# Kernel tuning notes

Hardware: AMD Instinct MI355X
Metric: run time of the kernel (lower is better)

## Reference

```python
import jax, jax.numpy as jnp
import numpy as np

IN_DIM = 256   # opt.word_vec_size
MEM_DIM = 256  # opt.rnn_size // num_directions
N_LEAVES = 131072  # 2**17, complete binary tree


def setup_inputs() -> dict:
    key = jax.random.key(0)
    ks = jax.random.split(key, 8)
    s = 0.05  # weight scale
    return {
        # leaf word2vec embeddings, in-order leaf sequence of the tree
        "x": jax.random.normal(ks[0], (N_LEAVES, IN_DIM), jnp.float32),
        # BinaryTreeLeafModule params (Linear as x @ W + b)
        "Wcx": jax.random.normal(ks[1], (IN_DIM, MEM_DIM), jnp.float32) * s,
        "bcx": jnp.zeros((MEM_DIM,), jnp.float32),
        "Wox": jax.random.normal(ks[2], (IN_DIM, MEM_DIM), jnp.float32) * s,
        "box": jnp.zeros((MEM_DIM,), jnp.float32),
        # BinaryTreeComposer params: 4 left-child gates (i, lf, rf, u) fused
        # along the output dim, likewise 4 right-child gates.
        "Wl": jax.random.normal(ks[3], (MEM_DIM, 4 * MEM_DIM), jnp.float32) * s,
        "bl": jnp.zeros((4 * MEM_DIM,), jnp.float32),
        "Wr": jax.random.normal(ks[4], (MEM_DIM, 4 * MEM_DIM), jnp.float32) * s,
        "br": jnp.zeros((4 * MEM_DIM,), jnp.float32),
        "lengths": N_LEAVES,  # max sequence length for output padding
    }


def reference(x, Wcx, bcx, Wox, box, Wl, bl, Wr, br, lengths):
    m = Wcx.shape[1]
    # ---- BinaryTreeLeafModule, batched over all leaves ----
    c = x @ Wcx + bcx                                   # [n, m]
    h = jax.nn.sigmoid(x @ Wox + box) * jnp.tanh(c)     # [n, m]
    leaf_h = h  # in-order cat of leaf outputs == recursive cat([lo, ro])

    # ---- BinaryTreeComposer, one batched step per tree level ----
    # Loop over log2(n_leaves) levels of a complete binary tree; each
    # iteration composes adjacent sibling pairs (shapes static -> jit-safe).
    while c.shape[0] > 1:
        lc, rc = c[0::2], c[1::2]
        lh, rh = h[0::2], h[1::2]
        g = (lh @ Wl + bl) + (rh @ Wr + br)             # [n/2, 4m]
        gi, glf, grf, gu = jnp.split(g, 4, axis=-1)
        i = jax.nn.sigmoid(gi)
        lf = jax.nn.sigmoid(glf)
        rf = jax.nn.sigmoid(grf)
        u = jnp.tanh(gu)
        c = i * u + lf * lc + rf * rc                   # [n/2, m]
        h = jnp.tanh(c)                                 # gate_output=False

    # ---- root post-processing (as in original when tree.parent is None) ----
    output = leaf_h[:, None, :]                         # [n_leaves, 1, m]
    supl = int(lengths) - output.shape[0]
    if supl > 0:
        output = jnp.concatenate(
            [output, jnp.zeros((supl, 1, m), output.dtype)], axis=0)
    c_root = c[:, None, :]                              # [1, 1, m]
    h_root = h[:, None, :]                              # [1, 1, m]
    return output, (c_root, h_root)
```

## Files before the change

kernel.cpp:

```cpp
#include <hip/hip_runtime.h>
#include <cstdint>
#include <cstddef>


typedef float floatx4 __attribute__((ext_vector_type(4)));
typedef __bf16 bf16x8 __attribute__((ext_vector_type(8)));

typedef __attribute__((address_space(1))) unsigned int u32g;
typedef __attribute__((address_space(3))) unsigned int u32l;

__device__ __forceinline__ void async_copy16(const void* g, void* l) {
  __builtin_amdgcn_global_load_lds((u32g*)(uintptr_t)g, (u32l*)l, 16, 0, 0);
}

__device__ __forceinline__ float sigf(float x) {
  return 1.f / (1.f + __expf(-x));
}
__device__ __forceinline__ float tanh_f(float x) {
  x = fminf(fmaxf(x, -15.f), 15.f);
  float e = __expf(2.f * x);
  return (e - 1.f) / (e + 1.f);
}

__global__ void prep_leaf(const float* __restrict__ Wcx, const float* __restrict__ bcx,
                          const float* __restrict__ Wox, const float* __restrict__ box,
                          __bf16* __restrict__ WleafT, float* __restrict__ bleaf) {
  int n = blockIdx.x;
  int k = threadIdx.x;
  const float* src = (n < 256) ? Wcx : Wox;
  int col = n & 255;
  WleafT[n * 256 + k] = (__bf16)src[k * 256 + col];
  if (k == 0) bleaf[n] = (n < 256) ? bcx[col] : box[col];
}

__global__ void prep_cat(const float* __restrict__ Wl, const float* __restrict__ bl,
                         const float* __restrict__ Wr, const float* __restrict__ br,
                         __bf16* __restrict__ WcatT, float* __restrict__ bcat) {
  int n = blockIdx.x;
  for (int k = threadIdx.x; k < 512; k += 256) {
    const float* src = (k < 256) ? Wl : Wr;
    WcatT[n * 512 + k] = (__bf16)src[(size_t)(k & 255) * 1024 + n];
  }
  if (threadIdx.x == 0) bcat[n] = bl[n] + br[n];
}

__global__ __launch_bounds__(256, 2) void leaf_kernel(
    const float* __restrict__ x,
    const __bf16* __restrict__ WT,
    const float* __restrict__ bleaf,
    __bf16* __restrict__ c_out,
    __bf16* __restrict__ h_out,
    float* __restrict__ h_out32)
{
  __shared__ __bf16 SMEM[16384];
  const int tid  = threadIdx.x;
  const int wave = tid >> 6;
  const int lane = tid & 63;
  const int quad = lane >> 4;
  const int l15  = lane & 15;

  const int lid = blockIdx.y * gridDim.x + blockIdx.x;
  const int nwg = gridDim.x * gridDim.y;
  const int swz = (lid & 7) * (nwg >> 3) + (lid >> 3);
  const int j0  = (swz & 3) * 64;
  const int bm  = swz >> 2;

  floatx4 acc[2][8];
#pragma unroll
  for (int r = 0; r < 2; ++r)
#pragma unroll
    for (int f = 0; f < 8; ++f) acc[r][f] = (floatx4){0.f, 0.f, 0.f, 0.f};

  for (int kk = 0; kk < 256; kk += 64) {
#pragma unroll
    for (int it = 0; it < 4; ++it) {
      int f = it * 256 + tid;
      int row = f >> 3, cc = f & 7;
      int cb = cc ^ (row & 7);
      const float4* gx = (const float4*)(x + (size_t)(bm * 128 + row) * 256 + kk + cc * 8);
      float4 u = gx[0], v = gx[1];
      bf16x8 a8 = {(__bf16)u.x, (__bf16)u.y, (__bf16)u.z, (__bf16)u.w,
                   (__bf16)v.x, (__bf16)v.y, (__bf16)v.z, (__bf16)v.w};
      *(bf16x8*)&SMEM[row * 64 + cb * 8] = a8;
      int ng = ((row >> 6) << 8) + j0 + (row & 63);
      async_copy16(WT + (size_t)ng * 256 + kk + cb * 8, &SMEM[8192 + (f & ~63) * 8]);
    }
    __syncthreads();
#pragma unroll
    for (int s = 0; s < 2; ++s) {
      const int b  = (s * 4 + quad) ^ (l15 & 7);
      const int kb = b * 8;
      bf16x8 a0 = *(const bf16x8*)&SMEM[(wave * 32 + l15) * 64 + kb];
      bf16x8 a1 = *(const bf16x8*)&SMEM[(wave * 32 + 16 + l15) * 64 + kb];
#pragma unroll
      for (int f = 0; f < 8; ++f) {
        bf16x8 b8 = *(const bf16x8*)&SMEM[8192 + (f * 16 + l15) * 64 + kb];
        acc[0][f] = __builtin_amdgcn_mfma_f32_16x16x32_bf16(a0, b8, acc[0][f], 0, 0, 0);
        acc[1][f] = __builtin_amdgcn_mfma_f32_16x16x32_bf16(a1, b8, acc[1][f], 0, 0, 0);
      }
    }
    __syncthreads();
  }

  float hv[2][4][4];
#pragma unroll
  for (int r = 0; r < 2; ++r) {
#pragma unroll
    for (int q = 0; q < 4; ++q) {
      int col = j0 + q * 16 + l15;
      float bC = bleaf[col];
      float bO = bleaf[256 + col];
#pragma unroll
      for (int reg = 0; reg < 4; ++reg) {
        int lr = wave * 32 + r * 16 + quad * 4 + reg;
        int lc = q * 16 + l15;
        float c = acc[r][q][reg] + bC;
        float o = acc[r][q + 4][reg] + bO;
        float h = sigf(o) * tanh_f(c);
        hv[r][q][reg] = h;
        int ch  = (lc >> 3) ^ ((lr ^ (lr >> 3)) & 7);
        int idx = lr * 64 + ch * 8 + (lc & 7);
        SMEM[idx]        = (__bf16)c;
        SMEM[8192 + idx] = (__bf16)h;
      }
    }
  }
  __syncthreads();
  const int R0 = bm * 128;
#pragma unroll
  for (int i = 0; i < 4; ++i) {
    int unit = i * 256 + tid;
    int lr = unit >> 3, k = unit & 7;
    int ch = k ^ ((lr ^ (lr >> 3)) & 7);
    bf16x8 vc = *(const bf16x8*)&SMEM[lr * 64 + ch * 8];
    bf16x8 vh = *(const bf16x8*)&SMEM[8192 + lr * 64 + ch * 8];
    size_t g = (size_t)(R0 + lr) * 256 + j0 + k * 8;
    *(bf16x8*)&c_out[g] = vc;
    *(bf16x8*)&h_out[g] = vh;
  }
  __syncthreads();
  float* Hf = (float*)SMEM;
#pragma unroll
  for (int r = 0; r < 2; ++r) {
#pragma unroll
    for (int q = 0; q < 4; ++q) {
#pragma unroll
      for (int reg = 0; reg < 4; ++reg) {
        int lr = wave * 32 + r * 16 + quad * 4 + reg;
        int lc = q * 16 + l15;
        int ph = ((lc >> 2) + lr) & 15;
        Hf[lr * 64 + ph * 4 + (lc & 3)] = hv[r][q][reg];
      }
    }
  }
  __syncthreads();
#pragma unroll
  for (int i = 0; i < 8; ++i) {
    int unit = i * 256 + tid;
    int lr = unit >> 4, k = unit & 15;
    int ph = (k + lr) & 15;
    float4 v = *(const float4*)&Hf[lr * 64 + ph * 4];
    *(float4*)&h_out32[(size_t)(R0 + lr) * 256 + j0 + k * 4] = v;
  }
}

template <typename OUT>
__global__ __launch_bounds__(256, 2) void tree_level(
    const __bf16* __restrict__ h_in,
    const __bf16* __restrict__ c_in,
    const __bf16* __restrict__ WT,
    const float* __restrict__ bcat,
    OUT* __restrict__ c_out,
    OUT* __restrict__ h_out,
    const int M)
{
  __shared__ __bf16 SMEM[16384];
  const int tid  = threadIdx.x;
  const int wave = tid >> 6;
  const int lane = tid & 63;
  const int quad = lane >> 4;
  const int l15  = lane & 15;

  const int lid = blockIdx.y * gridDim.x + blockIdx.x;
  const int nwg = gridDim.x * gridDim.y;
  const int swz = (lid & 7) * (nwg >> 3) + (lid >> 3);
  const int j0  = (swz & 7) * 32;
  const int bm  = swz >> 3;

  floatx4 acc[2][8];
#pragma unroll
  for (int r = 0; r < 2; ++r)
#pragma unroll
    for (int f = 0; f < 8; ++f) acc[r][f] = (floatx4){0.f, 0.f, 0.f, 0.f};

  for (int kk = 0; kk < 512; kk += 64) {
#pragma unroll
    for (int it = 0; it < 4; ++it) {
      int f = it * 256 + tid;
      int row = f >> 3, cc = f & 7;
      int cb = cc ^ (row & 7);
      int rg = bm * 128 + row;
      rg = rg < M ? rg : M - 1;
      async_copy16(h_in + (size_t)rg * 512 + kk + cb * 8, &SMEM[(f & ~63) * 8]);
      int ng = ((row >> 5) << 8) + j0 + (row & 31);
      async_copy16(WT + (size_t)ng * 512 + kk + cb * 8, &SMEM[8192 + (f & ~63) * 8]);
    }
    __syncthreads();
#pragma unroll
    for (int s = 0; s < 2; ++s) {
      const int b  = (s * 4 + quad) ^ (l15 & 7);
      const int kb = b * 8;
      bf16x8 a0 = *(const bf16x8*)&SMEM[(wave * 32 + l15) * 64 + kb];
      bf16x8 a1 = *(const bf16x8*)&SMEM[(wave * 32 + 16 + l15) * 64 + kb];
#pragma unroll
      for (int f = 0; f < 8; ++f) {
        bf16x8 b8 = *(const bf16x8*)&SMEM[8192 + (f * 16 + l15) * 64 + kb];
        acc[0][f] = __builtin_amdgcn_mfma_f32_16x16x32_bf16(a0, b8, acc[0][f], 0, 0, 0);
        acc[1][f] = __builtin_amdgcn_mfma_f32_16x16x32_bf16(a1, b8, acc[1][f], 0, 0, 0);
      }
    }
    __syncthreads();
  }

  if constexpr (sizeof(OUT) == 2) {
#pragma unroll
    for (int r = 0; r < 2; ++r) {
#pragma unroll
      for (int q = 0; q < 2; ++q) {
        int col = j0 + q * 16 + l15;
        float bi  = bcat[col];
        float blf = bcat[256 + col];
        float brf = bcat[512 + col];
        float bu  = bcat[768 + col];
#pragma unroll
        for (int reg = 0; reg < 4; ++reg) {
          int row = bm * 128 + wave * 32 + r * 16 + quad * 4 + reg;
          float cn = 0.f, hn = 0.f;
          if (row < M) {
            float lc = (float)c_in[(size_t)(2 * row) * 256 + col];
            float rc = (float)c_in[(size_t)(2 * row + 1) * 256 + col];
            float iv = sigf(acc[r][0 + q][reg] + bi);
            float lf = sigf(acc[r][2 + q][reg] + blf);
            float rf = sigf(acc[r][4 + q][reg] + brf);
            float uv = tanh_f(acc[r][6 + q][reg] + bu);
            cn = iv * uv + lf * lc + rf * rc;
            hn = tanh_f(cn);
          }
          int lr  = wave * 32 + r * 16 + quad * 4 + reg;
          int lcc = q * 16 + l15;
          int ch  = (lcc >> 3) ^ ((lr ^ (lr >> 2)) & 3);
          int idx = lr * 32 + ch * 8 + (lcc & 7);
          SMEM[idx]        = (__bf16)cn;
          SMEM[4096 + idx] = (__bf16)hn;
        }
      }
    }
    __syncthreads();
#pragma unroll
    for (int i = 0; i < 2; ++i) {
      int unit = i * 256 + tid;
      int lr = unit >> 2, k = unit & 3;
      int gr = bm * 128 + lr;
      if (gr < M) {
        int ch = k ^ ((lr ^ (lr >> 2)) & 3);
        bf16x8 vc = *(const bf16x8*)&SMEM[lr * 32 + ch * 8];
        bf16x8 vh = *(const bf16x8*)&SMEM[4096 + lr * 32 + ch * 8];
        size_t g = (size_t)gr * 256 + j0 + k * 8;
        *(bf16x8*)((__bf16*)c_out + g) = vc;
        *(bf16x8*)((__bf16*)h_out + g) = vh;
      }
    }
  } else {
#pragma unroll
    for (int r = 0; r < 2; ++r) {
#pragma unroll
      for (int q = 0; q < 2; ++q) {
        int col = j0 + q * 16 + l15;
        float bi  = bcat[col];
        float blf = bcat[256 + col];
        float brf = bcat[512 + col];
        float bu  = bcat[768 + col];
#pragma unroll
        for (int reg = 0; reg < 4; ++reg) {
          int row = bm * 128 + wave * 32 + r * 16 + quad * 4 + reg;
          if (row < M) {
            float lc = (float)c_in[(size_t)(2 * row) * 256 + col];
            float rc = (float)c_in[(size_t)(2 * row + 1) * 256 + col];
            float iv = sigf(acc[r][0 + q][reg] + bi);
            float lf = sigf(acc[r][2 + q][reg] + blf);
            float rf = sigf(acc[r][4 + q][reg] + brf);
            float uv = tanh_f(acc[r][6 + q][reg] + bu);
            float cn = iv * uv + lf * lc + rf * rc;
            float hn = tanh_f(cn);
            size_t idx = (size_t)row * 256 + col;
            c_out[idx] = (OUT)cn;
            h_out[idx] = (OUT)hn;
          }
        }
      }
    }
  }
}

extern "C" void kernel_launch(void* const* d_in, const int* in_sizes, int n_in,
                              void* d_out, int out_size, void* d_ws, size_t ws_size,
                              hipStream_t stream) {
  const float* x   = (const float*)d_in[0];
  const float* Wcx = (const float*)d_in[1];
  const float* bcx = (const float*)d_in[2];
  const float* Wox = (const float*)d_in[3];
  const float* box = (const float*)d_in[4];
  const float* Wl  = (const float*)d_in[5];
  const float* bl  = (const float*)d_in[6];
  const float* Wr  = (const float*)d_in[7];
  const float* br  = (const float*)d_in[8];

  const size_t LEAF = (size_t)131072 * 256;
  const size_t MiB  = 1ull << 20;
  char* ws = (char*)d_ws;

  __bf16* WleafT = (__bf16*)(ws);
  __bf16* WcatT  = (__bf16*)(ws + 262144);
  float*  bleaf  = (float*)(ws + 262144 + 1048576);
  float*  bcat   = bleaf + 512;

  int slog = 17;
  while (slog > 11) {
    size_t need = 2 * MiB + ((size_t)1 << slog) * 1792 + 65536;
    if (need <= ws_size) break;
    --slog;
  }
  const int SLAB  = 1 << slog;
  const int nslab = 131072 >> slog;

  char*   dyn    = ws + 2 * MiB;
  __bf16* LC     = (__bf16*)dyn;
  __bf16* LH     = LC + (size_t)SLAB * 256;
  char*   RA     = (char*)(LH + (size_t)SLAB * 256);
  char*   RB     = RA + (size_t)SLAB * 512;
  __bf16* rootsC = (__bf16*)(RB + (size_t)SLAB * 256);
  __bf16* rootsH = rootsC + (size_t)nslab * 256;

  float* out    = (float*)d_out;
  float* leaf_h = out;
  float* c_root = out + LEAF;
  float* h_root = out + LEAF + 256;

  prep_leaf<<<dim3(512), dim3(256), 0, stream>>>(Wcx, bcx, Wox, box, WleafT, bleaf);
  prep_cat<<<dim3(1024), dim3(256), 0, stream>>>(Wl, bl, Wr, br, WcatT, bcat);

  for (int sl = 0; sl < nslab; ++sl) {
    const size_t R0 = (size_t)sl * SLAB;
    leaf_kernel<<<dim3(4, SLAB / 128), dim3(256), 0, stream>>>(
        x + R0 * 256, WleafT, bleaf, LC, LH, leaf_h + R0 * 256);

    const __bf16* hin = LH;
    const __bf16* cin = LC;
    for (int lvl = 1; lvl <= slog; ++lvl) {
      const int M = SLAB >> lvl;
      dim3 grid(8, (M + 127) / 128);
      if (lvl == slog && nslab == 1) {
        tree_level<float><<<grid, dim3(256), 0, stream>>>(
            hin, cin, WcatT, bcat, c_root, h_root, M);
      } else {
        __bf16* cdst;
        if (lvl == slog) cdst = rootsC + (size_t)sl * 256;
        else             cdst = (__bf16*)((lvl & 1) ? RA : RB);
        __bf16* hdst = (lvl == slog) ? rootsH + (size_t)sl * 256
                                     : cdst + (size_t)M * 256;
        tree_level<__bf16><<<grid, dim3(256), 0, stream>>>(
            hin, cin, WcatT, bcat, cdst, hdst, M);
        hin = hdst; cin = cdst;
      }
    }
  }

  if (nslab > 1) {
    const __bf16* hin = rootsH;
    const __bf16* cin = rootsC;
    int pp = 1;
    for (int M = nslab / 2; M >= 1; M >>= 1, pp ^= 1) {
      if (M == 1) {
        tree_level<float><<<dim3(8, 1), dim3(256), 0, stream>>>(
            hin, cin, WcatT, bcat, c_root, h_root, 1);
      } else {
        __bf16* cdst = (__bf16*)(pp ? RA : RB);
        __bf16* hdst = cdst + (size_t)M * 256;
        tree_level<__bf16><<<dim3(8, 1), dim3(256), 0, stream>>>(
            hin, cin, WcatT, bcat, cdst, hdst, M);
        hin = hdst; cin = cdst;
      }
    }
  }
}
```

Measured before the change: 700.3 us.

## Stop per-slab tree at 1024 roots and batch upper levels across slabs

Each slab now reduces only down to 1024 nodes, collecting them into a shared buffer. The remaining upper levels then run once over all slabs together, which gives those launches wider grids than the old per-slab tail and the 8x1-grid root pass. The leaf kernel also writes fp32 h straight from registers instead of staging it through shared memory, which drops two barriers but makes the global stores less coalesced. Launch bounds rise to 4 waves per SIMD, which can force register spills.

```diff
diff --git a/kernel.cpp b/kernel.cpp
--- a/kernel.cpp
+++ b/kernel.cpp
@@ -44,7 +44,7 @@
   if (threadIdx.x == 0) bcat[n] = bl[n] + br[n];
 }
 
-__global__ __launch_bounds__(256, 2) void leaf_kernel(
+__global__ __launch_bounds__(256, 4) void leaf_kernel(
     const float* __restrict__ x,
     const __bf16* __restrict__ WT,
     const float* __restrict__ bleaf,
@@ -102,7 +102,7 @@
     __syncthreads();
   }
 
-  float hv[2][4][4];
+  const int R0 = bm * 128;
 #pragma unroll
   for (int r = 0; r < 2; ++r) {
 #pragma unroll
@@ -117,7 +117,7 @@
         float c = acc[r][q][reg] + bC;
         float o = acc[r][q + 4][reg] + bO;
         float h = sigf(o) * tanh_f(c);
-        hv[r][q][reg] = h;
+        h_out32[(size_t)(R0 + lr) * 256 + col] = h;
         int ch  = (lc >> 3) ^ ((lr ^ (lr >> 3)) & 7);
         int idx = lr * 64 + ch * 8 + (lc & 7);
         SMEM[idx]        = (__bf16)c;
@@ -126,7 +126,6 @@
     }
   }
   __syncthreads();
-  const int R0 = bm * 128;
 #pragma unroll
   for (int i = 0; i < 4; ++i) {
     int unit = i * 256 + tid;
@@ -138,34 +137,10 @@
     *(bf16x8*)&c_out[g] = vc;
     *(bf16x8*)&h_out[g] = vh;
   }
-  __syncthreads();
-  float* Hf = (float*)SMEM;
-#pragma unroll
-  for (int r = 0; r < 2; ++r) {
-#pragma unroll
-    for (int q = 0; q < 4; ++q) {
-#pragma unroll
-      for (int reg = 0; reg < 4; ++reg) {
-        int lr = wave * 32 + r * 16 + quad * 4 + reg;
-        int lc = q * 16 + l15;
-        int ph = ((lc >> 2) + lr) & 15;
-        Hf[lr * 64 + ph * 4 + (lc & 3)] = hv[r][q][reg];
-      }
-    }
-  }
-  __syncthreads();
-#pragma unroll
-  for (int i = 0; i < 8; ++i) {
-    int unit = i * 256 + tid;
-    int lr = unit >> 4, k = unit & 15;
-    int ph = (k + lr) & 15;
-    float4 v = *(const float4*)&Hf[lr * 64 + ph * 4];
-    *(float4*)&h_out32[(size_t)(R0 + lr) * 256 + j0 + k * 4] = v;
-  }
 }
 
 template <typename OUT>
-__global__ __launch_bounds__(256, 2) void tree_level(
+__global__ __launch_bounds__(256, 4) void tree_level(
     const __bf16* __restrict__ h_in,
     const __bf16* __restrict__ c_in,
     const __bf16* __restrict__ WT,
@@ -325,21 +300,26 @@
   float*  bcat   = bleaf + 512;
 
   int slog = 17;
+  size_t ra_sz = 0, rb_sz = 0;
   while (slog > 11) {
-    size_t need = 2 * MiB + ((size_t)1 << slog) * 1792 + 65536;
+    size_t SL  = (size_t)1 << slog;
+    size_t nsl = (size_t)(131072 >> slog);
+    ra_sz = SL * 512 > nsl * 524288 ? SL * 512 : nsl * 524288;
+    rb_sz = SL * 256 > nsl * 262144 ? SL * 256 : nsl * 262144;
+    size_t need = 2 * MiB + SL * 1024 + ra_sz + rb_sz + nsl * MiB;
     if (need <= ws_size) break;
     --slog;
   }
   const int SLAB  = 1 << slog;
   const int nslab = 131072 >> slog;
 
-  char*   dyn    = ws + 2 * MiB;
-  __bf16* LC     = (__bf16*)dyn;
-  __bf16* LH     = LC + (size_t)SLAB * 256;
-  char*   RA     = (char*)(LH + (size_t)SLAB * 256);
-  char*   RB     = RA + (size_t)SLAB * 512;
-  __bf16* rootsC = (__bf16*)(RB + (size_t)SLAB * 256);
-  __bf16* rootsH = rootsC + (size_t)nslab * 256;
+  char*   dyn = ws + 2 * MiB;
+  __bf16* LC  = (__bf16*)dyn;
+  __bf16* LH  = LC + (size_t)SLAB * 256;
+  char*   RA  = (char*)(LH + (size_t)SLAB * 256);
+  char*   RB  = RA + ra_sz;
+  __bf16* CC  = (__bf16*)(RB + rb_sz);
+  __bf16* CH  = CC + (size_t)nslab * 1024 * 256;
 
   float* out    = (float*)d_out;
   float* leaf_h = out;
@@ -349,6 +329,7 @@
   prep_leaf<<<dim3(512), dim3(256), 0, stream>>>(Wcx, bcx, Wox, box, WleafT, bleaf);
   prep_cat<<<dim3(1024), dim3(256), 0, stream>>>(Wl, bl, Wr, br, WcatT, bcat);
 
+  const int STOP = slog - 10;
   for (int sl = 0; sl < nslab; ++sl) {
     const size_t R0 = (size_t)sl * SLAB;
     leaf_kernel<<<dim3(4, SLAB / 128), dim3(256), 0, stream>>>(
@@ -356,37 +337,36 @@
 
     const __bf16* hin = LH;
     const __bf16* cin = LC;
-    for (int lvl = 1; lvl <= slog; ++lvl) {
+    for (int lvl = 1; lvl <= STOP; ++lvl) {
       const int M = SLAB >> lvl;
       dim3 grid(8, (M + 127) / 128);
-      if (lvl == slog && nslab == 1) {
+      __bf16 *cdst, *hdst;
+      if (lvl == STOP) {
+        cdst = CC + (size_t)sl * 1024 * 256;
+        hdst = CH + (size_t)sl * 1024 * 256;
+      } else {
+        cdst = (__bf16*)((lvl & 1) ? RA : RB);
+        hdst = cdst + (size_t)M * 256;
+      }
+      tree_level<__bf16><<<grid, dim3(256), 0, stream>>>(
+          hin, cin, WcatT, bcat, cdst, hdst, M);
+      hin = hdst; cin = cdst;
+    }
+  }
+
+  {
+    const __bf16* hin = CH;
+    const __bf16* cin = CC;
+    int pp = 1;
+    for (int M = (nslab << 10) >> 1; M >= 1; M >>= 1, pp ^= 1) {
+      dim3 grid(8, (M + 127) / 128);
+      if (M == 1) {
         tree_level<float><<<grid, dim3(256), 0, stream>>>(
-            hin, cin, WcatT, bcat, c_root, h_root, M);
-      } else {
-        __bf16* cdst;
-        if (lvl == slog) cdst = rootsC + (size_t)sl * 256;
-        else             cdst = (__bf16*)((lvl & 1) ? RA : RB);
-        __bf16* hdst = (lvl == slog) ? rootsH + (size_t)sl * 256
-                                     : cdst + (size_t)M * 256;
-        tree_level<__bf16><<<grid, dim3(256), 0, stream>>>(
-            hin, cin, WcatT, bcat, cdst, hdst, M);
-        hin = hdst; cin = cdst;
-      }
-    }
-  }
-
-  if (nslab > 1) {
-    const __bf16* hin = rootsH;
-    const __bf16* cin = rootsC;
-    int pp = 1;
-    for (int M = nslab / 2; M >= 1; M >>= 1, pp ^= 1) {
-      if (M == 1) {
-        tree_level<float><<<dim3(8, 1), dim3(256), 0, stream>>>(
             hin, cin, WcatT, bcat, c_root, h_root, 1);
       } else {
         __bf16* cdst = (__bf16*)(pp ? RA : RB);
         __bf16* hdst = cdst + (size_t)M * 256;
-        tree_level<__bf16><<<dim3(8, 1), dim3(256), 0, stream>>>(
+        tree_level<__bf16><<<grid, dim3(256), 0, stream>>>(
             hin, cin, WcatT, bcat, cdst, hdst, M);
         hin = hdst; cin = cdst;
       }
```

Result: slower. 715.5 us (+2.2%).
